# Kernel tuning notes

Measured on AMD Instinct MI355X. Metric: run time of the kernel, lower is better.

## Reference

```python
import jax, jax.numpy as jnp
import numpy as np

D_MODEL = 1024
N_HEAD = 16
D_HEAD = D_MODEL // N_HEAD
NEG = -1e9


def setup_inputs() -> dict:
    key = jax.random.key(0)
    ks = jax.random.split(key, 11)
    B, T, C = 4, 2048, D_MODEL
    s = 1.0 / np.sqrt(C)
    return {
        "q": jax.random.normal(ks[0], (B, T, C), jnp.float32),
        "k": jax.random.normal(ks[1], (B, T, C), jnp.float32),
        "v": jax.random.normal(ks[2], (B, T, C), jnp.float32),
        "w_q": jax.random.normal(ks[3], (C, C), jnp.float32) * s,
        "b_q": jnp.zeros((C,), jnp.float32),
        "w_k": jax.random.normal(ks[4], (C, C), jnp.float32) * s,
        "b_k": jnp.zeros((C,), jnp.float32),
        "w_v": jax.random.normal(ks[5], (C, C), jnp.float32) * s,
        "b_v": jnp.zeros((C,), jnp.float32),
        "w_o": jax.random.normal(ks[6], (C, C), jnp.float32) * s,
        "b_o": jnp.zeros((C,), jnp.float32),
    }


def reference(q, k, v, w_q, b_q, w_k, b_k, w_v, b_v, w_o, b_o):
    B, T, C = q.shape
    # projections; weights stored as [in, out]
    qh = (q @ w_q + b_q).reshape(B, T, N_HEAD, D_HEAD).transpose(0, 2, 1, 3)
    kh = (k @ w_k + b_k).reshape(B, T, N_HEAD, D_HEAD).transpose(0, 2, 1, 3)
    vh = (v @ w_v + b_v).reshape(B, T, N_HEAD, D_HEAD).transpose(0, 2, 1, 3)
    scores = jnp.einsum("bhqd,bhkd->bhqk", qh, kh) / jnp.sqrt(
        jnp.asarray(D_HEAD, qh.dtype))
    causal = jnp.tril(jnp.ones((T, T), dtype=bool))  # [T,T]
    scores = jnp.where(causal[None, None], scores, NEG)
    attn = jax.nn.softmax(scores, axis=-1)
    out = jnp.einsum("bhqk,bhkd->bhqd", attn, vh)
    out = out.transpose(0, 2, 1, 3).reshape(B, T, C)
    return out @ w_o + b_o
```

## Files before the change

kernel.cpp:

```cpp
#include <hip/hip_runtime.h>
#include <hip/hip_bf16.h>
#include <cstdint>
#include <cstddef>

#define DEVI static __device__ __forceinline__

typedef __attribute__((ext_vector_type(8))) short short8;
typedef __attribute__((ext_vector_type(4))) float f32x4;

typedef __attribute__((address_space(1))) const unsigned int as1c_uint;
typedef __attribute__((address_space(3))) unsigned int as3_uint;

constexpr int Bn = 4, Tn = 2048, Cn = 1024, Hn = 16, Dn = 64;
constexpr int Mtot = Bn * Tn;
#define QSCALE (0.125f * 1.44269504088896340736f)

DEVI unsigned short f2bf(float f) {
  unsigned u = __float_as_uint(f);
  u += 0x7fffu + ((u >> 16) & 1u);
  return (unsigned short)(u >> 16);
}
DEVI unsigned short f2bf_t(float f) {
  return (unsigned short)(__float_as_uint(f) >> 16);
}

DEVI void async16(const void* g, void* l) {
  __builtin_amdgcn_global_load_lds((as1c_uint*)g, (as3_uint*)l, 16, 0, 0);
}

__global__ __launch_bounds__(256) void transpose_cvt4(
    const float* __restrict__ w0, const float* __restrict__ w1,
    const float* __restrict__ w2, const float* __restrict__ w3,
    unsigned short* __restrict__ o0, unsigned short* __restrict__ o1,
    unsigned short* __restrict__ o2, unsigned short* __restrict__ o3) {
  __shared__ float tile[32][33];
  const int z = blockIdx.z;
  const float* w = z == 0 ? w0 : z == 1 ? w1 : z == 2 ? w2 : w3;
  unsigned short* wT = z == 0 ? o0 : z == 1 ? o1 : z == 2 ? o2 : o3;
  int n0 = blockIdx.x * 32, k0 = blockIdx.y * 32;
  int tx = threadIdx.x, ty = threadIdx.y;
#pragma unroll
  for (int r = 0; r < 32; r += 8)
    tile[ty + r][tx] = w[(size_t)(k0 + ty + r) * Cn + n0 + tx];
  __syncthreads();
  const int t = ty * 32 + tx;
  const int n_l = t >> 3;
  const int kq = (t & 7) * 4;
  const int n = n0 + n_l, k = k0 + kq;
  ushort4 pk;
#pragma unroll
  for (int e = 0; e < 4; ++e) ((unsigned short*)&pk)[e] = f2bf(tile[kq + e][n_l]);
  size_t idx = (size_t)((((n >> 4) * 32 + (k >> 5)) * 64 + ((k >> 3) & 3) * 16 + (n & 15))) * 8 + (k & 7);
  *(ushort4*)&wT[idx] = pk;
}

DEVI short8 xfrag(const unsigned short* Xlds, int i, int kc, int l15, int l4) {
  int row = i * 16 + l15;
  return *(const short8*)&Xlds[row * 1024 + (((kc * 4 + l4) ^ (row & 7)) * 8)];
}

template <int IB, int NJ, bool SWAP>
DEVI void proj_core(const unsigned short* __restrict__ wF,
                    const unsigned short* Xlds, int njb, int lane,
                    f32x4 (&acc)[IB][NJ]) {
  const int l15 = lane & 15, l4 = lane >> 4;
  constexpr int H = NJ / 2;
  const short8* wp = (const short8*)wF;
  short8 wfc[H], wfn[H];
#pragma unroll
  for (int h = 0; h < H; ++h) wfc[h] = wp[(size_t)((njb + h) * 32) * 64 + lane];
#pragma unroll 1
  for (int kc = 0; kc < 32; ++kc) {
#pragma unroll
    for (int h = 0; h < H; ++h)
      wfn[h] = wp[(size_t)((njb + H + h) * 32 + kc) * 64 + lane];
    short8 xf[IB];
#pragma unroll
    for (int i = 0; i < IB; ++i) xf[i] = xfrag(Xlds, i, kc, l15, l4);
#pragma unroll
    for (int i = 0; i < IB; ++i)
#pragma unroll
      for (int h = 0; h < H; ++h)
        acc[i][h] = SWAP
            ? __builtin_amdgcn_mfma_f32_16x16x32_bf16(xf[i], wfc[h], acc[i][h], 0, 0, 0)
            : __builtin_amdgcn_mfma_f32_16x16x32_bf16(wfc[h], xf[i], acc[i][h], 0, 0, 0);
    if (kc + 1 < 32) {
#pragma unroll
      for (int h = 0; h < H; ++h)
        wfc[h] = wp[(size_t)((njb + h) * 32 + kc + 1) * 64 + lane];
    }
#pragma unroll
    for (int i = 0; i < IB; ++i)
#pragma unroll
      for (int h = 0; h < H; ++h)
        acc[i][H + h] = SWAP
            ? __builtin_amdgcn_mfma_f32_16x16x32_bf16(xf[i], wfn[h], acc[i][H + h], 0, 0, 0)
            : __builtin_amdgcn_mfma_f32_16x16x32_bf16(wfn[h], xf[i], acc[i][H + h], 0, 0, 0);
  }
}

DEVI void stage64_f32(const float* __restrict__ src, int m0,
                      unsigned short* Xlds, int tid) {
#pragma unroll
  for (int it = 0; it < 8; ++it) {
    int g = it * 1024 + tid;
    int row = g >> 7, slot = g & 127;
    const float4* p = (const float4*)(src + (size_t)(m0 + row) * Cn + slot * 8);
    float4 a = p[0], b = p[1];
    short8 sv;
    sv[0] = (short)f2bf(a.x); sv[1] = (short)f2bf(a.y);
    sv[2] = (short)f2bf(a.z); sv[3] = (short)f2bf(a.w);
    sv[4] = (short)f2bf(b.x); sv[5] = (short)f2bf(b.y);
    sv[6] = (short)f2bf(b.z); sv[7] = (short)f2bf(b.w);
    *(short8*)&Xlds[row * 1024 + ((slot ^ (row & 7)) * 8)] = sv;
  }
}

DEVI void stage32_bf(const unsigned short* __restrict__ src, int m0,
                     unsigned short* Xlds, int tid) {
#pragma unroll
  for (int it = 0; it < 8; ++it) {
    int s = it * 512 + tid;
    int row = s >> 7, sl = s & 127;
    async16(src + (size_t)(m0 + row) * Cn + ((sl ^ (row & 7)) * 8),
            Xlds + (size_t)(it * 512 + (tid & ~63)) * 8);
  }
}

__global__ __launch_bounds__(1024, 4) void proj_qkv(
    const float* __restrict__ xqf, const float* __restrict__ xkf,
    const float* __restrict__ xvf, const unsigned short* __restrict__ wFq,
    const unsigned short* __restrict__ wFk, const unsigned short* __restrict__ wFv,
    const float* __restrict__ bq, const float* __restrict__ bk,
    const float* __restrict__ bv, unsigned short* __restrict__ oq,
    unsigned short* __restrict__ ok, unsigned short* __restrict__ ov) {
  __shared__ unsigned short Xlds[64 * 1024];
  const int tid = threadIdx.x, lane = tid & 63, w = tid >> 6;
  const int l15 = lane & 15, l4 = lane >> 4;
  const int bid = blockIdx.x;
  const int z = bid >> 7;
  const int m0 = (bid & 127) * 64;
  const float* xz = z == 0 ? xqf : z == 1 ? xkf : xvf;
  const unsigned short* wF = z == 0 ? wFq : z == 1 ? wFk : wFv;
  const float* bias = z == 0 ? bq : z == 1 ? bk : bv;

  stage64_f32(xz, m0, Xlds, tid);
  __syncthreads();

  const f32x4 zf = {0.f, 0.f, 0.f, 0.f};
  f32x4 acc[4][4];
#pragma unroll
  for (int i = 0; i < 4; ++i)
#pragma unroll
    for (int j = 0; j < 4; ++j) acc[i][j] = zf;

  const int njb = w * 4;
  if (z < 2)
    proj_core<4, 4, false>(wF, Xlds, njb, lane, acc);
  else
    proj_core<4, 4, true>(wF, Xlds, njb, lane, acc);

  const int b = m0 >> 11, t0loc = m0 & 2047;
  if (z < 2) {
    unsigned short* o = z == 0 ? oq : ok;
    const float scale = z == 0 ? QSCALE : 1.f;
#pragma unroll
    for (int j = 0; j < 4; ++j) {
      int ng = njb + j;
      int h = ng >> 2, d0 = (ng & 3) * 16 + l4 * 4;
      float4 bv4 = *(const float4*)&bias[ng * 16 + l4 * 4];
#pragma unroll
      for (int i = 0; i < 4; ++i) {
        int t = t0loc + i * 16 + l15;
        ushort4 pk;
        pk.x = f2bf((acc[i][j][0] + bv4.x) * scale);
        pk.y = f2bf((acc[i][j][1] + bv4.y) * scale);
        pk.z = f2bf((acc[i][j][2] + bv4.z) * scale);
        pk.w = f2bf((acc[i][j][3] + bv4.w) * scale);
        *(ushort4*)&o[((size_t)((b * Hn + h) * Tn + t)) * Dn + d0] = pk;
      }
    }
  } else {
#pragma unroll
    for (int j = 0; j < 4; ++j) {
      int n = (njb + j) * 16 + l15;
      int h = n >> 6, d = n & 63;
      float bvl = bias[n];
#pragma unroll
      for (int i = 0; i < 4; ++i) {
        int t0 = t0loc + i * 16 + l4 * 4;
        ushort4 pk;
        pk.x = f2bf(acc[i][j][0] + bvl);
        pk.y = f2bf(acc[i][j][1] + bvl);
        pk.z = f2bf(acc[i][j][2] + bvl);
        pk.w = f2bf(acc[i][j][3] + bvl);
        *(ushort4*)&ov[((size_t)((b * Hn + h) * Dn + d)) * Tn + t0] = pk;
      }
    }
  }
}

__global__ __launch_bounds__(512, 4) void proj_out(
    const unsigned short* __restrict__ A, const unsigned short* __restrict__ wFo,
    const float* __restrict__ bias, float* __restrict__ o) {
  __shared__ unsigned short Xlds[32 * 1024];
  const int tid = threadIdx.x, lane = tid & 63, w = tid >> 6;
  const int l15 = lane & 15, l4 = lane >> 4;
  const int bid = blockIdx.x;
  const int m0 = (bid >> 1) * 32, nh = bid & 1;

  stage32_bf(A, m0, Xlds, tid);
  __syncthreads();

  const f32x4 zf = {0.f, 0.f, 0.f, 0.f};
  f32x4 acc[2][4];
#pragma unroll
  for (int i = 0; i < 2; ++i)
#pragma unroll
    for (int j = 0; j < 4; ++j) acc[i][j] = zf;

  const int njb = nh * 32 + w * 4;
  proj_core<2, 4, false>(wFo, Xlds, njb, lane, acc);

#pragma unroll
  for (int j = 0; j < 4; ++j) {
    int ng = njb + j;
    float4 bv4 = *(const float4*)&bias[ng * 16 + l4 * 4];
#pragma unroll
    for (int i = 0; i < 2; ++i) {
      int m = m0 + i * 16 + l15;
      float4 ov4;
      ov4.x = acc[i][j][0] + bv4.x;
      ov4.y = acc[i][j][1] + bv4.y;
      ov4.z = acc[i][j][2] + bv4.z;
      ov4.w = acc[i][j][3] + bv4.w;
      *(float4*)&o[(size_t)m * Cn + ng * 16 + l4 * 4] = ov4;
    }
  }
}

__global__ __launch_bounds__(512) void attn_kernel(const unsigned short* __restrict__ qh,
                                                   const unsigned short* __restrict__ kh,
                                                   const unsigned short* __restrict__ vt,
                                                   unsigned short* __restrict__ obf) {
  __shared__ unsigned short Ks[2][64 * 64];
  __shared__ unsigned short Vs[2][64 * 64];
  __shared__ unsigned short Ps[8][16 * 72];

  const int tid = threadIdx.x, lane = tid & 63, w = tid >> 6;
  const int l15 = lane & 15, l4 = lane >> 4;
  const int swz = l15 & 7;

  const int bid = blockIdx.x;
  const int j = bid >> 3;
  const int bh = (bid & 7) * 8 + (j & 7);
  const int pair = j >> 3;
  const unsigned short* qb = qh + (size_t)bh * Tn * Dn;
  const unsigned short* kb = kh + (size_t)bh * Tn * Dn;
  const unsigned short* vb = vt + (size_t)bh * Dn * Tn;
  const int b = bh >> 4, h = bh & 15;

  const int srow = lane >> 3, sslot = (lane & 7) ^ (lane >> 3);

  const f32x4 z = {0.f, 0.f, 0.f, 0.f};
  const short ob = (short)0x3F80;
  const short8 ones = {ob, ob, ob, ob, ob, ob, ob, ob};

#pragma unroll 1
  for (int half = 0; half < 2; ++half) {
    const int qt = half == 0 ? pair : 15 - pair;
    const int q0 = qt * 128;
    const int qrow = q0 + w * 16 + l15;

    short8 qf0 = *(const short8*)(qb + (size_t)qrow * Dn + l4 * 8);
    short8 qf1 = *(const short8*)(qb + (size_t)qrow * Dn + 32 + l4 * 8);

    f32x4 o[4];
#pragma unroll
    for (int nd = 0; nd < 4; ++nd) o[nd] = z;
    f32x4 osum = z;

    const int nt = (q0 >> 6) + 2;
    const int ntw = ((q0 + w * 16 + 15) >> 6) + 1;

    {
      const unsigned short* ksrc = kb + (size_t)(w * 8 + srow) * Dn + sslot * 8;
      const unsigned short* vsrc = vb + (size_t)(w * 8 + srow) * Tn + sslot * 8;
      async16(ksrc, &Ks[0][w * 512]);
      async16(vsrc, &Vs[0][w * 512]);
    }

#pragma unroll 1
    for (int t = 0; t < nt; ++t) {
      const int cur = t & 1;
      if (t + 1 < nt) {
        const int kv1 = (t + 1) * 64;
        const unsigned short* ksrc = kb + (size_t)(kv1 + w * 8 + srow) * Dn + sslot * 8;
        const unsigned short* vsrc = vb + (size_t)(w * 8 + srow) * Tn + kv1 + sslot * 8;
        async16(ksrc, &Ks[cur ^ 1][w * 512]);
        async16(vsrc, &Vs[cur ^ 1][w * 512]);
        asm volatile("s_waitcnt vmcnt(2)" ::: "memory");
      } else {
        asm volatile("s_waitcnt vmcnt(0)" ::: "memory");
      }
      __builtin_amdgcn_s_barrier();
      __builtin_amdgcn_sched_barrier(0);

      if (t < ntw) {
        const unsigned short* Kc = &Ks[cur][0];
        const unsigned short* Vc = &Vs[cur][0];

        f32x4 s[4];
#pragma unroll
        for (int ni = 0; ni < 4; ++ni) s[ni] = z;
        __builtin_amdgcn_s_setprio(1);
#pragma unroll
        for (int ni = 0; ni < 4; ++ni) {
          const int rb = (ni * 16 + l15) * 64;
          short8 kf0 = *(const short8*)&Kc[rb + ((l4 ^ swz) * 8)];
          short8 kf1 = *(const short8*)&Kc[rb + (((4 + l4) ^ swz) * 8)];
          s[ni] = __builtin_amdgcn_mfma_f32_16x16x32_bf16(kf0, qf0, s[ni], 0, 0, 0);
          s[ni] = __builtin_amdgcn_mfma_f32_16x16x32_bf16(kf1, qf1, s[ni], 0, 0, 0);
        }
        __builtin_amdgcn_s_setprio(0);

        short8 vf[8];
#pragma unroll
        for (int nd = 0; nd < 4; ++nd) {
          const int rb = (nd * 16 + l15) * 64;
          vf[nd * 2]     = *(const short8*)&Vc[rb + ((l4 ^ swz) * 8)];
          vf[nd * 2 + 1] = *(const short8*)&Vc[rb + (((4 + l4) ^ swz) * 8)];
        }

        const int kq = qrow - t * 64;
        const bool edge = (t * 64 + 63 > q0 + w * 16);
        if (!edge) {
#pragma unroll
          for (int ni = 0; ni < 4; ++ni) {
            ushort4 pk;
#pragma unroll
            for (int r = 0; r < 4; ++r)
              ((unsigned short*)&pk)[r] = f2bf_t(__builtin_amdgcn_exp2f(s[ni][r]));
            *(ushort4*)&Ps[w][l15 * 72 + ni * 16 + l4 * 4] = pk;
          }
        } else {
#pragma unroll
          for (int ni = 0; ni < 4; ++ni) {
            ushort4 pk;
#pragma unroll
            for (int r = 0; r < 4; ++r) {
              float e = __builtin_amdgcn_exp2f(s[ni][r]);
              if ((ni * 16 + l4 * 4 + r) > kq) e = 0.f;
              ((unsigned short*)&pk)[r] = f2bf_t(e);
            }
            *(ushort4*)&Ps[w][l15 * 72 + ni * 16 + l4 * 4] = pk;
          }
        }
        asm volatile("s_waitcnt lgkmcnt(0)" ::: "memory");
        __builtin_amdgcn_sched_barrier(0);

        short8 pf0 = *(const short8*)&Ps[w][l15 * 72 + l4 * 8];
        short8 pf1 = *(const short8*)&Ps[w][l15 * 72 + 32 + l4 * 8];
        __builtin_amdgcn_s_setprio(1);
        osum = __builtin_amdgcn_mfma_f32_16x16x32_bf16(pf0, ones, osum, 0, 0, 0);
        osum = __builtin_amdgcn_mfma_f32_16x16x32_bf16(pf1, ones, osum, 0, 0, 0);
#pragma unroll
        for (int nd = 0; nd < 4; ++nd) {
          o[nd] = __builtin_amdgcn_mfma_f32_16x16x32_bf16(pf0, vf[nd * 2], o[nd], 0, 0, 0);
          o[nd] = __builtin_amdgcn_mfma_f32_16x16x32_bf16(pf1, vf[nd * 2 + 1], o[nd], 0, 0, 0);
        }
        __builtin_amdgcn_s_setprio(0);
      }

      __builtin_amdgcn_sched_barrier(0);
      __builtin_amdgcn_s_barrier();
    }

#pragma unroll
    for (int r = 0; r < 4; ++r) {
      float inv = __builtin_amdgcn_rcpf(osum[r]);
      int tq = q0 + w * 16 + l4 * 4 + r;
      size_t base = ((size_t)(b * Tn + tq)) * Cn + h * 64;
#pragma unroll
      for (int nd = 0; nd < 4; ++nd)
        obf[base + nd * 16 + l15] = f2bf(o[nd][r] * inv);
    }
  }
}

extern "C" void kernel_launch(void* const* d_in, const int* in_sizes, int n_in,
                              void* d_out, int out_size, void* d_ws, size_t ws_size,
                              hipStream_t stream) {
  const float* q   = (const float*)d_in[0];
  const float* k   = (const float*)d_in[1];
  const float* v   = (const float*)d_in[2];
  const float* w_q = (const float*)d_in[3];
  const float* b_q = (const float*)d_in[4];
  const float* w_k = (const float*)d_in[5];
  const float* b_k = (const float*)d_in[6];
  const float* w_v = (const float*)d_in[7];
  const float* b_v = (const float*)d_in[8];
  const float* w_o = (const float*)d_in[9];
  const float* b_o = (const float*)d_in[10];

  char* ws = (char*)d_ws;
  const size_t MB = 1u << 20;
  unsigned short* qhp  = (unsigned short*)(ws);
  unsigned short* khp  = (unsigned short*)(ws + 16 * MB);
  unsigned short* vtp  = (unsigned short*)(ws + 32 * MB);
  unsigned short* aout = (unsigned short*)(ws + 48 * MB);
  unsigned short* wqT  = (unsigned short*)(ws + 64 * MB);
  unsigned short* wkT  = (unsigned short*)(ws + 66 * MB);
  unsigned short* wvT  = (unsigned short*)(ws + 68 * MB);
  unsigned short* woT  = (unsigned short*)(ws + 70 * MB);

  transpose_cvt4<<<dim3(32, 32, 4), dim3(32, 8), 0, stream>>>(
      w_q, w_k, w_v, w_o, wqT, wkT, wvT, woT);

  proj_qkv<<<384, 1024, 0, stream>>>(q, k, v, wqT, wkT, wvT,
                                     b_q, b_k, b_v, qhp, khp, vtp);

  attn_kernel<<<512, 512, 0, stream>>>(qhp, khp, vtp, aout);

  proj_out<<<512, 512, 0, stream>>>(aout, woT, b_o, (float*)d_out);
}
```

Before: 165.2 us.

## Retile projection GEMMs: split QKV over column halves, enlarge out-proj row tile

The QKV projection now splits each 64-row block across two column halves, doubling the grid to 768 blocks, and each wave computes 2 column tiles instead of 4. The output projection moves from 32-row, 512-thread blocks to 64-row, 1024-thread blocks with a 4x2 accumulator layout, halving its grid to 256. The MFMA inner loop is restructured to double-buffer weight fragments across consecutive k-chunks rather than across column halves. The aim is better CU occupancy for the QKV GEMM and more weight reuse per block in the output GEMM. The cost is that QKV activations are staged and converted twice, and proj_out has fewer blocks.

```diff
diff --git a/kernel.cpp b/kernel.cpp
--- a/kernel.cpp
+++ b/kernel.cpp
@@ -64,38 +64,39 @@
                     const unsigned short* Xlds, int njb, int lane,
                     f32x4 (&acc)[IB][NJ]) {
   const int l15 = lane & 15, l4 = lane >> 4;
-  constexpr int H = NJ / 2;
   const short8* wp = (const short8*)wF;
-  short8 wfc[H], wfn[H];
-#pragma unroll
-  for (int h = 0; h < H; ++h) wfc[h] = wp[(size_t)((njb + h) * 32) * 64 + lane];
+  short8 wfA[NJ], wfB[NJ];
+#pragma unroll
+  for (int j = 0; j < NJ; ++j) wfA[j] = wp[(size_t)((njb + j) * 32) * 64 + lane];
 #pragma unroll 1
-  for (int kc = 0; kc < 32; ++kc) {
-#pragma unroll
-    for (int h = 0; h < H; ++h)
-      wfn[h] = wp[(size_t)((njb + H + h) * 32 + kc) * 64 + lane];
+  for (int kc = 0; kc < 32; kc += 2) {
+#pragma unroll
+    for (int j = 0; j < NJ; ++j)
+      wfB[j] = wp[(size_t)((njb + j) * 32 + kc + 1) * 64 + lane];
     short8 xf[IB];
 #pragma unroll
     for (int i = 0; i < IB; ++i) xf[i] = xfrag(Xlds, i, kc, l15, l4);
 #pragma unroll
     for (int i = 0; i < IB; ++i)
 #pragma unroll
-      for (int h = 0; h < H; ++h)
-        acc[i][h] = SWAP
-            ? __builtin_amdgcn_mfma_f32_16x16x32_bf16(xf[i], wfc[h], acc[i][h], 0, 0, 0)
-            : __builtin_amdgcn_mfma_f32_16x16x32_bf16(wfc[h], xf[i], acc[i][h], 0, 0, 0);
-    if (kc + 1 < 32) {
-#pragma unroll
-      for (int h = 0; h < H; ++h)
-        wfc[h] = wp[(size_t)((njb + h) * 32 + kc + 1) * 64 + lane];
-    }
+      for (int j = 0; j < NJ; ++j)
+        acc[i][j] = SWAP
+            ? __builtin_amdgcn_mfma_f32_16x16x32_bf16(xf[i], wfA[j], acc[i][j], 0, 0, 0)
+            : __builtin_amdgcn_mfma_f32_16x16x32_bf16(wfA[j], xf[i], acc[i][j], 0, 0, 0);
+    if (kc + 2 < 32) {
+#pragma unroll
+      for (int j = 0; j < NJ; ++j)
+        wfA[j] = wp[(size_t)((njb + j) * 32 + kc + 2) * 64 + lane];
+    }
+#pragma unroll
+    for (int i = 0; i < IB; ++i) xf[i] = xfrag(Xlds, i, kc + 1, l15, l4);
 #pragma unroll
     for (int i = 0; i < IB; ++i)
 #pragma unroll
-      for (int h = 0; h < H; ++h)
-        acc[i][H + h] = SWAP
-            ? __builtin_amdgcn_mfma_f32_16x16x32_bf16(xf[i], wfn[h], acc[i][H + h], 0, 0, 0)
-            : __builtin_amdgcn_mfma_f32_16x16x32_bf16(wfn[h], xf[i], acc[i][H + h], 0, 0, 0);
+      for (int j = 0; j < NJ; ++j)
+        acc[i][j] = SWAP
+            ? __builtin_amdgcn_mfma_f32_16x16x32_bf16(xf[i], wfB[j], acc[i][j], 0, 0, 0)
+            : __builtin_amdgcn_mfma_f32_16x16x32_bf16(wfB[j], xf[i], acc[i][j], 0, 0, 0);
   }
 }
 
@@ -116,14 +117,14 @@
   }
 }
 
-DEVI void stage32_bf(const unsigned short* __restrict__ src, int m0,
+DEVI void stage64_bf(const unsigned short* __restrict__ src, int m0,
                      unsigned short* Xlds, int tid) {
 #pragma unroll
   for (int it = 0; it < 8; ++it) {
-    int s = it * 512 + tid;
+    int s = it * 1024 + tid;
     int row = s >> 7, sl = s & 127;
     async16(src + (size_t)(m0 + row) * Cn + ((sl ^ (row & 7)) * 8),
-            Xlds + (size_t)(it * 512 + (tid & ~63)) * 8);
+            Xlds + (size_t)(it * 1024 + (tid & ~63)) * 8);
   }
 }
 
@@ -138,8 +139,10 @@
   const int tid = threadIdx.x, lane = tid & 63, w = tid >> 6;
   const int l15 = lane & 15, l4 = lane >> 4;
   const int bid = blockIdx.x;
-  const int z = bid >> 7;
-  const int m0 = (bid & 127) * 64;
+  const int z = bid >> 8;
+  const int r = bid & 255;
+  const int m0 = (r >> 1) * 64;
+  const int nh = r & 1;
   const float* xz = z == 0 ? xqf : z == 1 ? xkf : xvf;
   const unsigned short* wF = z == 0 ? wFq : z == 1 ? wFk : wFv;
   const float* bias = z == 0 ? bq : z == 1 ? bk : bv;
@@ -148,24 +151,24 @@
   __syncthreads();
 
   const f32x4 zf = {0.f, 0.f, 0.f, 0.f};
-  f32x4 acc[4][4];
+  f32x4 acc[4][2];
 #pragma unroll
   for (int i = 0; i < 4; ++i)
 #pragma unroll
-    for (int j = 0; j < 4; ++j) acc[i][j] = zf;
-
-  const int njb = w * 4;
+    for (int j = 0; j < 2; ++j) acc[i][j] = zf;
+
+  const int njb = nh * 32 + w * 2;
   if (z < 2)
-    proj_core<4, 4, false>(wF, Xlds, njb, lane, acc);
+    proj_core<4, 2, false>(wF, Xlds, njb, lane, acc);
   else
-    proj_core<4, 4, true>(wF, Xlds, njb, lane, acc);
+    proj_core<4, 2, true>(wF, Xlds, njb, lane, acc);
 
   const int b = m0 >> 11, t0loc = m0 & 2047;
   if (z < 2) {
     unsigned short* o = z == 0 ? oq : ok;
     const float scale = z == 0 ? QSCALE : 1.f;
 #pragma unroll
-    for (int j = 0; j < 4; ++j) {
+    for (int j = 0; j < 2; ++j) {
       int ng = njb + j;
       int h = ng >> 2, d0 = (ng & 3) * 16 + l4 * 4;
       float4 bv4 = *(const float4*)&bias[ng * 16 + l4 * 4];
@@ -182,7 +185,7 @@
     }
   } else {
 #pragma unroll
-    for (int j = 0; j < 4; ++j) {
+    for (int j = 0; j < 2; ++j) {
       int n = (njb + j) * 16 + l15;
       int h = n >> 6, d = n & 63;
       float bvl = bias[n];
@@ -200,34 +203,34 @@
   }
 }
 
-__global__ __launch_bounds__(512, 4) void proj_out(
+__global__ __launch_bounds__(1024, 4) void proj_out(
     const unsigned short* __restrict__ A, const unsigned short* __restrict__ wFo,
     const float* __restrict__ bias, float* __restrict__ o) {
-  __shared__ unsigned short Xlds[32 * 1024];
+  __shared__ unsigned short Xlds[64 * 1024];
   const int tid = threadIdx.x, lane = tid & 63, w = tid >> 6;
   const int l15 = lane & 15, l4 = lane >> 4;
   const int bid = blockIdx.x;
-  const int m0 = (bid >> 1) * 32, nh = bid & 1;
-
-  stage32_bf(A, m0, Xlds, tid);
+  const int m0 = (bid >> 1) * 64, nh = bid & 1;
+
+  stage64_bf(A, m0, Xlds, tid);
   __syncthreads();
 
   const f32x4 zf = {0.f, 0.f, 0.f, 0.f};
-  f32x4 acc[2][4];
-#pragma unroll
-  for (int i = 0; i < 2; ++i)
-#pragma unroll
-    for (int j = 0; j < 4; ++j) acc[i][j] = zf;
-
-  const int njb = nh * 32 + w * 4;
-  proj_core<2, 4, false>(wFo, Xlds, njb, lane, acc);
-
-#pragma unroll
-  for (int j = 0; j < 4; ++j) {
+  f32x4 acc[4][2];
+#pragma unroll
+  for (int i = 0; i < 4; ++i)
+#pragma unroll
+    for (int j = 0; j < 2; ++j) acc[i][j] = zf;
+
+  const int njb = nh * 32 + w * 2;
+  proj_core<4, 2, false>(wFo, Xlds, njb, lane, acc);
+
+#pragma unroll
+  for (int j = 0; j < 2; ++j) {
     int ng = njb + j;
     float4 bv4 = *(const float4*)&bias[ng * 16 + l4 * 4];
 #pragma unroll
-    for (int i = 0; i < 2; ++i) {
+    for (int i = 0; i < 4; ++i) {
       int m = m0 + i * 16 + l15;
       float4 ov4;
       ov4.x = acc[i][j][0] + bv4.x;
@@ -417,10 +420,10 @@
   transpose_cvt4<<<dim3(32, 32, 4), dim3(32, 8), 0, stream>>>(
       w_q, w_k, w_v, w_o, wqT, wkT, wvT, woT);
 
-  proj_qkv<<<384, 1024, 0, stream>>>(q, k, v, wqT, wkT, wvT,
+  proj_qkv<<<768, 1024, 0, stream>>>(q, k, v, wqT, wkT, wvT,
                                      b_q, b_k, b_v, qhp, khp, vtp);
 
   attn_kernel<<<512, 512, 0, stream>>>(qhp, khp, vtp, aout);
 
-  proj_out<<<512, 512, 0, stream>>>(aout, woT, b_o, (float*)d_out);
-}
+  proj_out<<<256, 1024, 0, stream>>>(aout, woT, b_o, (float*)d_out);
+}
```

Result: slower. 169.1 us (+2.4%).
